# Performance work log

Measured on AMD Instinct MI355X. Metric: run time of the kernel, lower is better.

Reference implementation:

```python
import jax, jax.numpy as jnp
import numpy as np

S, T, B, E, H, V = 64, 64, 64, 256, 256, 32000
PAD = 0


def _lstm_layer(X, Wih, Whh, b, h0, c0):
    # X: (time, B, in), torch gate order i,f,g,o
    def step(carry, x_t):
        h, c = carry
        z = x_t @ Wih.T + h @ Whh.T + b
        i, f, g, o = jnp.split(z, 4, axis=-1)
        c = jax.nn.sigmoid(f) * c + jax.nn.sigmoid(i) * jnp.tanh(g)
        h = jax.nn.sigmoid(o) * jnp.tanh(c)
        return (h, c), h
    (hT, cT), outs = jax.lax.scan(step, (h0, c0), X)
    return outs, hT, cT


def setup_inputs() -> dict:
    key = jax.random.key(0)
    ks = jax.random.split(key, 20)
    p = lambda k, shape: (jax.random.normal(k, shape, jnp.float32) * 0.05)
    inp = {
        "source_padded": jax.random.randint(ks[0], (S, B), 0, V, jnp.int32),
        "target_padded": jax.random.randint(ks[1], (T, B), 0, V, jnp.int32),
        "src_emb": p(ks[2], (V, E)),
        "tgt_emb": p(ks[3], (V, E)),
        "enc_Wih_f": p(ks[4], (4 * H, E)),
        "enc_Whh_f": p(ks[5], (4 * H, H)),
        "enc_b_f": p(ks[6], (4 * H,)),
        "enc_Wih_b": p(ks[7], (4 * H, E)),
        "enc_Whh_b": p(ks[8], (4 * H, H)),
        "enc_b_b": p(ks[9], (4 * H,)),
        "dec_Wih": p(ks[10], (4 * H, E + H)),
        "dec_Whh": p(ks[11], (4 * H, H)),
        "dec_b": p(ks[12], (4 * H,)),
        "Wh": p(ks[13], (H, 2 * H)),
        "Wc": p(ks[14], (H, 2 * H)),
        "Watt": p(ks[15], (H, 2 * H)),
        "Wcomb": p(ks[16], (H, 3 * H)),
        "Wvocab": p(ks[17], (V, H)),
    }
    return inp


def reference(source_padded, target_padded, src_emb, tgt_emb,
              enc_Wih_f, enc_Whh_f, enc_b_f, enc_Wih_b, enc_Whh_b, enc_b_b,
              dec_Wih, dec_Whh, dec_b, Wh, Wc, Watt, Wcomb, Wvocab):
    X = src_emb[source_padded]                      # (S,B,E)
    h0 = jnp.zeros((B, H), X.dtype)
    c0 = jnp.zeros((B, H), X.dtype)
    # bidirectional encoder (all sequences full length -> pack is identity)
    fwd_out, hf, cf = _lstm_layer(X, enc_Wih_f, enc_Whh_f, enc_b_f, h0, c0)
    bwd_out, hb, cb = _lstm_layer(X[::-1], enc_Wih_b, enc_Whh_b, enc_b_b, h0, c0)
    bwd_out = bwd_out[::-1]
    enc_hiddens = jnp.concatenate([fwd_out, bwd_out], -1).transpose(1, 0, 2)  # (B,S,2H)
    dec_h = jnp.concatenate([hf, hb], -1) @ Wh.T     # h_projection
    dec_c = jnp.concatenate([cf, cb], -1) @ Wc.T     # c_projection
    enc_proj = enc_hiddens @ Watt.T                  # (B,S,H)

    Y = tgt_emb[target_padded[:-1]]                  # (T-1,B,E)

    def dstep(carry, Y_t):
        h, c, o_prev = carry
        x = jnp.concatenate([Y_t, o_prev], -1)       # (B,E+H)
        z = x @ dec_Wih.T + h @ dec_Whh.T + dec_b
        i, f, g, o = jnp.split(z, 4, axis=-1)
        c = jax.nn.sigmoid(f) * c + jax.nn.sigmoid(i) * jnp.tanh(g)
        h = jax.nn.sigmoid(o) * jnp.tanh(c)
        e_t = jnp.einsum('bsh,bh->bs', enc_proj, h)  # attention scores
        alpha = jax.nn.softmax(e_t, axis=-1)         # no pads -> mask is no-op
        a_t = jnp.einsum('bs,bsd->bd', alpha, enc_hiddens)  # context (B,2H)
        O_t = jnp.tanh(jnp.concatenate([a_t, h], -1) @ Wcomb.T)  # dropout=eval
        return (h, c, O_t), O_t

    _, outs = jax.lax.scan(dstep, (dec_h, dec_c, jnp.zeros((B, H), X.dtype)), Y)
    P = jax.nn.log_softmax(outs @ Wvocab.T, axis=-1)          # (T-1,B,V)
    gold = jnp.take_along_axis(P, target_padded[1:][..., None], axis=-1)[..., 0]
    tmask = (target_padded[1:] != PAD).astype(P.dtype)
    return (gold * tmask).sum(axis=0)                          # (B,)
```

## Files before the change

kernel.cpp:

```cpp
#include <hip/hip_runtime.h>
#include <hip/hip_bf16.h>

static constexpr int S = 64, T = 64, B = 64, E = 256, H = 256, V = 32000;
static constexpr int H4 = 4 * H;
static constexpr int NCHUNK = 500;
static constexpr int NROW = (T - 1) * B;
static constexpr int LDP = 264;

typedef short bf16x8 __attribute__((ext_vector_type(8)));
typedef float f32x4 __attribute__((ext_vector_type(4)));
typedef unsigned long long ull;

__device__ __forceinline__ float sigf(float x) { return 1.0f / (1.0f + __expf(-x)); }
__device__ __forceinline__ float tanhfast(float x) { return 1.0f - 2.0f / (__expf(2.0f * x) + 1.0f); }
__device__ __forceinline__ float bflo(uint w) { return __uint_as_float(w << 16); }
__device__ __forceinline__ float bfhi(uint w) { return __uint_as_float(w & 0xffff0000u); }
__device__ __forceinline__ ushort f2bu(float x) {
  return __bfloat16_as_ushort(__float2bfloat16(x));
}
__device__ __forceinline__ uint packbf(float a, float b) {
  return (uint)f2bu(a) | ((uint)f2bu(b) << 16);
}

__device__ __forceinline__ void st_u32(uint* p, uint v) {
  __hip_atomic_store(p, v, __ATOMIC_RELAXED, __HIP_MEMORY_SCOPE_AGENT);
}
__device__ __forceinline__ uint ld_u32(const uint* p) {
  return __hip_atomic_load(p, __ATOMIC_RELAXED, __HIP_MEMORY_SCOPE_AGENT);
}

__global__ __launch_bounds__(256) void k_gemm_gather(
    const int* __restrict__ idx, const float* __restrict__ emb,
    const float* __restrict__ W, int wld, const float* __restrict__ bias,
    float* __restrict__ C, int ldc) {
  __shared__ __align__(16) ushort Asl[64 * LDP];
  __shared__ __align__(16) ushort Bsl[64 * LDP];
  const int cb = blockIdx.x * 64, rb = blockIdx.y * 64;
  const int tid = threadIdx.x;
  const int lane = tid & 63, wid = tid >> 6;
  const int wr = wid >> 1, wc = wid & 1;
  const int l15 = lane & 15, l4 = lane >> 4;
  for (int it = 0; it < 8; it++) {
    int c = it * 256 + tid;
    int row = c >> 5, off = (c & 31) * 8;
    const float* asrc = emb + (size_t)idx[rb + row] * 256 + off;
    float4 a0 = *(const float4*)asrc;
    float4 a1 = *(const float4*)(asrc + 4);
    uint4 av;
    av.x = packbf(a0.x, a0.y); av.y = packbf(a0.z, a0.w);
    av.z = packbf(a1.x, a1.y); av.w = packbf(a1.z, a1.w);
    *(uint4*)&Asl[row * LDP + off] = av;
    const float* bsrc = W + (size_t)(cb + row) * wld + off;
    float4 b0 = *(const float4*)bsrc;
    float4 b1 = *(const float4*)(bsrc + 4);
    uint4 bv;
    bv.x = packbf(b0.x, b0.y); bv.y = packbf(b0.z, b0.w);
    bv.z = packbf(b1.x, b1.y); bv.w = packbf(b1.z, b1.w);
    *(uint4*)&Bsl[row * LDP + off] = bv;
  }
  __syncthreads();
  f32x4 acc[2][2];
  #pragma unroll
  for (int m = 0; m < 2; m++)
    #pragma unroll
    for (int n = 0; n < 2; n++) acc[m][n] = (f32x4){0.f, 0.f, 0.f, 0.f};
  for (int kk = 0; kk < 8; kk++) {
    int ko = kk * 32 + l4 * 8;
    bf16x8 a0 = *(const bf16x8*)&Asl[(wr * 32 + l15) * LDP + ko];
    bf16x8 a1 = *(const bf16x8*)&Asl[(wr * 32 + 16 + l15) * LDP + ko];
    bf16x8 b0 = *(const bf16x8*)&Bsl[(wc * 32 + l15) * LDP + ko];
    bf16x8 b1 = *(const bf16x8*)&Bsl[(wc * 32 + 16 + l15) * LDP + ko];
    acc[0][0] = __builtin_amdgcn_mfma_f32_16x16x32_bf16(a0, b0, acc[0][0], 0, 0, 0);
    acc[0][1] = __builtin_amdgcn_mfma_f32_16x16x32_bf16(a0, b1, acc[0][1], 0, 0, 0);
    acc[1][0] = __builtin_amdgcn_mfma_f32_16x16x32_bf16(a1, b0, acc[1][0], 0, 0, 0);
    acc[1][1] = __builtin_amdgcn_mfma_f32_16x16x32_bf16(a1, b1, acc[1][1], 0, 0, 0);
  }
  #pragma unroll
  for (int m = 0; m < 2; m++)
    #pragma unroll
    for (int n = 0; n < 2; n++) {
      int col = cb + wc * 32 + n * 16 + l15;
      float bv = bias[col];
      #pragma unroll
      for (int r = 0; r < 4; r++) {
        int row = rb + wr * 32 + m * 16 + l4 * 4 + r;
        C[(size_t)row * ldc + col] = acc[m][n][r] + bv;
      }
    }
}

__global__ __launch_bounds__(256) void k_encproj_mfma(
    const __hip_bfloat16* __restrict__ fwd_bf, const __hip_bfloat16* __restrict__ bwd_bf,
    const __hip_bfloat16* __restrict__ Watt_bf, __hip_bfloat16* __restrict__ encproj_bf) {
  __shared__ __align__(16) ushort Asl[64 * LDP];
  __shared__ __align__(16) ushort Bsl[64 * LDP];
  const int cb = blockIdx.x * 64, rb = blockIdx.y * 64;
  const int tid = threadIdx.x;
  const int lane = tid & 63, wid = tid >> 6;
  const int wr = wid >> 1, wc = wid & 1;
  const int l15 = lane & 15, l4 = lane >> 4;
  f32x4 acc[2][2];
  #pragma unroll
  for (int m = 0; m < 2; m++)
    #pragma unroll
    for (int n = 0; n < 2; n++) acc[m][n] = (f32x4){0.f, 0.f, 0.f, 0.f};
  for (int kt = 0; kt < 2; kt++) {
    if (kt) __syncthreads();
    for (int it = 0; it < 8; it++) {
      int c = it * 256 + tid;
      int row = c >> 5, off = (c & 31) * 8;
      int r = rb + row, s = r >> 6, bb = r & 63;
      const ushort* arow = (kt == 0)
          ? (const ushort*)fwd_bf + (size_t)(s * 64 + bb) * 256
          : (const ushort*)bwd_bf + (size_t)(s * 64 + bb) * 256;
      *(uint4*)&Asl[row * LDP + off] = *(const uint4*)(arow + off);
      *(uint4*)&Bsl[row * LDP + off] =
          *(const uint4*)((const ushort*)Watt_bf + (size_t)(cb + row) * 512 + kt * 256 + off);
    }
    __syncthreads();
    for (int kk = 0; kk < 8; kk++) {
      int ko = kk * 32 + l4 * 8;
      bf16x8 a0 = *(const bf16x8*)&Asl[(wr * 32 + l15) * LDP + ko];
      bf16x8 a1 = *(const bf16x8*)&Asl[(wr * 32 + 16 + l15) * LDP + ko];
      bf16x8 b0 = *(const bf16x8*)&Bsl[(wc * 32 + l15) * LDP + ko];
      bf16x8 b1 = *(const bf16x8*)&Bsl[(wc * 32 + 16 + l15) * LDP + ko];
      acc[0][0] = __builtin_amdgcn_mfma_f32_16x16x32_bf16(a0, b0, acc[0][0], 0, 0, 0);
      acc[0][1] = __builtin_amdgcn_mfma_f32_16x16x32_bf16(a0, b1, acc[0][1], 0, 0, 0);
      acc[1][0] = __builtin_amdgcn_mfma_f32_16x16x32_bf16(a1, b0, acc[1][0], 0, 0, 0);
      acc[1][1] = __builtin_amdgcn_mfma_f32_16x16x32_bf16(a1, b1, acc[1][1], 0, 0, 0);
    }
  }
  #pragma unroll
  for (int m = 0; m < 2; m++)
    #pragma unroll
    for (int n = 0; n < 2; n++) {
      int col = cb + wc * 32 + n * 16 + l15;
      #pragma unroll
      for (int r = 0; r < 4; r++) {
        int row = rb + wr * 32 + m * 16 + l4 * 4 + r;
        int s = row >> 6, bb = row & 63;
        ((ushort*)encproj_bf)[(size_t)(bb * 64 + s) * 256 + col] = f2bu(acc[m][n][r]);
      }
    }
}

__global__ __launch_bounds__(256) void k_vocab2(
    const uint* __restrict__ outs_u, const __hip_bfloat16* __restrict__ Wv,
    const int* __restrict__ tgt, float* __restrict__ part_max,
    float* __restrict__ part_sum, float* __restrict__ gold) {
  __shared__ __align__(16) ushort Asl[64 * LDP];
  __shared__ __align__(16) ushort Bsl[64 * LDP];
  __shared__ int goldcol[64];
  __shared__ float pm[64][2], ps[64][2];
  const int vb = blockIdx.x;
  const int tid = threadIdx.x;
  const int lane = tid & 63, wid = tid >> 6;
  const int wr = wid >> 1, wc = wid & 1;
  const int l15 = lane & 15, l4 = lane >> 4;
  for (int it = 0; it < 8; it++) {
    int c = it * 256 + tid;
    int row = c >> 5, off = (c & 31) * 8;
    *(uint4*)&Bsl[row * LDP + off] =
        *(const uint4*)((const ushort*)Wv + (size_t)(vb * 64 + row) * 256 + off);
  }
  for (int t = 0; t < T - 1; t++) {
    __syncthreads();
    for (int i = tid; i < 64 * 128; i += 256) {
      int row = i >> 7, colu = i & 127;
      uint v = outs_u[(size_t)(t * 64 + row) * 128 + colu];
      *(uint*)&Asl[row * LDP + colu * 2] = v;
    }
    if (tid < 64) goldcol[tid] = tgt[(t + 1) * B + tid];
    __syncthreads();
    f32x4 acc[2][2];
    #pragma unroll
    for (int m = 0; m < 2; m++)
      #pragma unroll
      for (int n = 0; n < 2; n++) acc[m][n] = (f32x4){0.f, 0.f, 0.f, 0.f};
    for (int kk = 0; kk < 8; kk++) {
      int ko = kk * 32 + l4 * 8;
      bf16x8 a0 = *(const bf16x8*)&Asl[(wr * 32 + l15) * LDP + ko];
      bf16x8 a1 = *(const bf16x8*)&Asl[(wr * 32 + 16 + l15) * LDP + ko];
      bf16x8 b0 = *(const bf16x8*)&Bsl[(wc * 32 + l15) * LDP + ko];
      bf16x8 b1 = *(const bf16x8*)&Bsl[(wc * 32 + 16 + l15) * LDP + ko];
      acc[0][0] = __builtin_amdgcn_mfma_f32_16x16x32_bf16(a0, b0, acc[0][0], 0, 0, 0);
      acc[0][1] = __builtin_amdgcn_mfma_f32_16x16x32_bf16(a0, b1, acc[0][1], 0, 0, 0);
      acc[1][0] = __builtin_amdgcn_mfma_f32_16x16x32_bf16(a1, b0, acc[1][0], 0, 0, 0);
      acc[1][1] = __builtin_amdgcn_mfma_f32_16x16x32_bf16(a1, b1, acc[1][1], 0, 0, 0);
    }
    #pragma unroll
    for (int m = 0; m < 2; m++) {
      #pragma unroll
      for (int r = 0; r < 4; r++) {
        int row_local = wr * 32 + m * 16 + l4 * 4 + r;
        int gc = goldcol[row_local];
        #pragma unroll
        for (int n = 0; n < 2; n++) {
          int col = vb * 64 + wc * 32 + n * 16 + l15;
          if (col == gc) gold[t * 64 + row_local] = acc[m][n][r];
        }
        float v = fmaxf(acc[m][0][r], acc[m][1][r]);
        #pragma unroll
        for (int o = 1; o < 16; o <<= 1) v = fmaxf(v, __shfl_xor(v, o));
        float e = __expf(acc[m][0][r] - v) + __expf(acc[m][1][r] - v);
        #pragma unroll
        for (int o = 1; o < 16; o <<= 1) e += __shfl_xor(e, o);
        if (l15 == 0) { pm[row_local][wc] = v; ps[row_local][wc] = e; }
      }
    }
    __syncthreads();
    if (tid < 64) {
      float m0 = pm[tid][0], m1 = pm[tid][1];
      float M = fmaxf(m0, m1);
      float Ss = ps[tid][0] * __expf(m0 - M) + ps[tid][1] * __expf(m1 - M);
      part_max[(size_t)vb * NROW + t * 64 + tid] = M;
      part_sum[(size_t)vb * NROW + t * 64 + tid] = Ss;
    }
  }
}

__global__ __launch_bounds__(256) void k_enc4w(
    const float* __restrict__ XwF, const float* __restrict__ XwB,
    const float* __restrict__ WhhF, const float* __restrict__ WhhB,
    uint* __restrict__ Xenc_u32,
    __hip_bfloat16* __restrict__ fwd_bf, __hip_bfloat16* __restrict__ bwd_bf,
    float* __restrict__ Cfin, uint* __restrict__ eflags,
    const float* __restrict__ Wv, __hip_bfloat16* __restrict__ Wv_bf,
    const float* __restrict__ Watt, __hip_bfloat16* __restrict__ Watt_bf,
    const float* __restrict__ Wcomb, uint2* __restrict__ Wcq) {
  __shared__ __align__(16) ushort Wl[128 * 264];
  __shared__ __align__(16) ushort Xa[16 * 264];
  __shared__ float zz[4][8][33];
  const int id = blockIdx.x;
  const int tid = threadIdx.x;
  if (id >= 128) {
    const int wtid = (id - 128) * 256 + tid;
    const int wn = 64 * 256;
    for (int i = wtid; i < (V * H) / 4; i += wn) {
      float4 v = ((const float4*)Wv)[i];
      uint2 o; o.x = packbf(v.x, v.y); o.y = packbf(v.z, v.w);
      ((uint2*)Wv_bf)[i] = o;
    }
    for (int i = wtid; i < (H * 512) / 4; i += wn) {
      float4 v = ((const float4*)Watt)[i];
      uint2 o; o.x = packbf(v.x, v.y); o.y = packbf(v.z, v.w);
      ((uint2*)Watt_bf)[i] = o;
    }
    for (int i2 = wtid; i2 < 192 * 256; i2 += wn) {
      int i = i2 >> 8, j = i2 & 255;
      float4 v = *(const float4*)(Wcomb + (size_t)j * 768 + 4 * i);
      uint2 o; o.x = packbf(v.x, v.y); o.y = packbf(v.z, v.w);
      Wcq[(size_t)i * 256 + j] = o;
    }
    return;
  }
  const int g = id & 7, kb = id >> 3;
  const int dir = kb >> 3, s = kb & 7;
  const float* Whh = dir ? WhhB : WhhF;
  const float* Xw = dir ? XwB : XwF;
  uint* fl = eflags + (size_t)(g * 2 + dir) * 8 * 32;
  for (int i = tid; i < 128 * 256; i += 256) {
    int c = i >> 8, k2 = i & 255;
    int gate = c >> 5, jj = c & 31;
    Wl[c * 264 + k2] = f2bu(Whh[(size_t)(gate * 256 + s * 32 + jj) * 256 + k2]);
  }
  for (int i = tid; i < 16 * 264; i += 256) Xa[i] = 0;
  const int lane = tid & 63, w = tid >> 6;
  const int l15 = lane & 15, l4 = lane >> 4;
  const int tb = tid >> 5, tjj = tid & 31;
  float c_reg = 0.f;
  __syncthreads();
  for (int st = 0; st < 64; st++) {
    const int ts = dir ? 63 - st : st;
    const int par = st & 1;
    const uint* Xr = Xenc_u32 + (size_t)(par * 2 + dir) * 8192;
    uint* Xo = Xenc_u32 + (size_t)((par ^ 1) * 2 + dir) * 8192;
    for (int i = tid; i < 8 * 128; i += 256) {
      int row = i >> 7, colu = i & 127;
      uint v = ld_u32(Xr + (size_t)(8 * g + row) * 128 + colu);
      *(uint*)&Xa[row * 264 + colu * 2] = v;
    }
    __syncthreads();
    f32x4 a0v = (f32x4){0.f, 0.f, 0.f, 0.f}, a1v = (f32x4){0.f, 0.f, 0.f, 0.f};
    for (int kk = 0; kk < 8; kk++) {
      bf16x8 af = *(const bf16x8*)&Xa[l15 * 264 + kk * 32 + l4 * 8];
      bf16x8 b0 = *(const bf16x8*)&Wl[((2 * w) * 16 + l15) * 264 + kk * 32 + l4 * 8];
      bf16x8 b1 = *(const bf16x8*)&Wl[((2 * w + 1) * 16 + l15) * 264 + kk * 32 + l4 * 8];
      a0v = __builtin_amdgcn_mfma_f32_16x16x32_bf16(af, b0, a0v, 0, 0, 0);
      a1v = __builtin_amdgcn_mfma_f32_16x16x32_bf16(af, b1, a1v, 0, 0, 0);
    }
    if (l4 < 2) {
      #pragma unroll
      for (int r = 0; r < 4; r++) {
        int b = l4 * 4 + r;
        zz[w][b][l15] = a0v[r];
        zz[w][b][16 + l15] = a1v[r];
      }
    }
    __syncthreads();
    {
      int gb = 8 * g + tb, j = 32 * s + tjj;
      const float* xw = Xw + (size_t)(ts * 64 + gb) * 1024;
      float zi = zz[0][tb][tjj] + xw[j];
      float zf = zz[1][tb][tjj] + xw[256 + j];
      float zg = zz[2][tb][tjj] + xw[512 + j];
      float zo = zz[3][tb][tjj] + xw[768 + j];
      float c = sigf(zf) * c_reg + sigf(zi) * tanhfast(zg);
      c_reg = c;
      float h = sigf(zo) * tanhfast(c);
      ushort hb = f2bu(h);
      if (dir == 0) ((ushort*)fwd_bf)[(size_t)(st * 64 + gb) * 256 + j] = hb;
      else          ((ushort*)bwd_bf)[(size_t)((63 - st) * 64 + gb) * 256 + j] = hb;
      float hp = __shfl_xor(h, 1);
      if ((tjj & 1) == 0)
        st_u32(Xo + (size_t)gb * 128 + 16 * s + (tjj >> 1), packbf(h, hp));
    }
    __syncthreads();
    if (tid == 0) st_u32(&fl[s * 32], (uint)(st + 1));
    if (tid < 8)
      while (ld_u32(&fl[tid * 32]) < (uint)(st + 1)) __builtin_amdgcn_s_sleep(2);
    asm volatile("" ::: "memory");
    __syncthreads();
  }
  Cfin[(size_t)(dir * 64 + 8 * g + tb) * 256 + 32 * s + tjj] = c_reg;
}

__global__ __launch_bounds__(256) void k_dec_init3(
    const __hip_bfloat16* __restrict__ Xenc, const float* __restrict__ Cfin,
    const float* __restrict__ Wh, const float* __restrict__ Wc,
    uint* __restrict__ Xd_u32, float* __restrict__ decc0) {
  int b = blockIdx.x, tid = threadIdx.x;
  __shared__ __align__(16) float ch[512], cc[512];
  __shared__ float hh[256];
  ch[tid]       = __bfloat162float(Xenc[(size_t)(0 * 64 + b) * 256 + tid]);
  ch[256 + tid] = __bfloat162float(Xenc[(size_t)(1 * 64 + b) * 256 + tid]);
  cc[tid]       = Cfin[(size_t)(0 * 64 + b) * 256 + tid];
  cc[256 + tid] = Cfin[(size_t)(1 * 64 + b) * 256 + tid];
  __syncthreads();
  const float* wh = Wh + tid * 512;
  const float* wc = Wc + tid * 512;
  float ah = 0, ac = 0;
  for (int k = 0; k < 512; k += 4) {
    float4 hv = *(const float4*)&ch[k];
    float4 cv = *(const float4*)&cc[k];
    float4 w1 = *(const float4*)&wh[k];
    float4 w2 = *(const float4*)&wc[k];
    ah += hv.x * w1.x + hv.y * w1.y + hv.z * w1.z + hv.w * w1.w;
    ac += cv.x * w2.x + cv.y * w2.y + cv.z * w2.z + cv.w * w2.w;
  }
  decc0[b * 256 + tid] = ac;
  hh[tid] = ah;
  __syncthreads();
  if (tid < 128) {
    Xd_u32[(size_t)b * 256 + tid] = packbf(hh[2 * tid], hh[2 * tid + 1]);
    Xd_u32[(size_t)b * 256 + 128 + tid] = 0u;
  }
}

__global__ __launch_bounds__(512) void k_dec6(
    const float* __restrict__ YW, const float* __restrict__ dWih,
    const float* __restrict__ dWhh, const uint2* __restrict__ Wcq,
    const __hip_bfloat16* __restrict__ encproj_bf,
    const __hip_bfloat16* __restrict__ fwd_bf, const __hip_bfloat16* __restrict__ bwd_bf,
    const float* __restrict__ decc0, uint* __restrict__ Xd_u32,
    uint* __restrict__ outs_u,
    uint* __restrict__ zflags, uint* __restrict__ aflags) {
  __shared__ __align__(16) char smem[154112];
  const int id = blockIdx.x;
  const int g = id & 7, kb = id >> 3;
  const int tid = threadIdx.x;
  uint* zfl = zflags + (size_t)g * 8 * 32;
  uint* afl = aflags + (size_t)g * 16 * 32;

  if (kb < 8) {
    const int s = kb;
    ushort* Wl = (ushort*)smem;
    ushort* Xa = (ushort*)(smem + 133120);
    float* zslds = (float*)(smem + 149760);
    for (int i = tid; i < 128 * 512; i += 512) {
      int c = i >> 9, k2 = i & 511;
      int gate = c >> 5, jj = c & 31;
      int gr = gate * 256 + 32 * s + jj;
      float v = (k2 < 256) ? dWhh[(size_t)gr * 256 + k2]
                           : dWih[(size_t)gr * 512 + 256 + (k2 - 256)];
      Wl[c * 520 + k2] = f2bu(v);
    }
    for (int i = tid; i < 16 * 520; i += 512) Xa[i] = 0;
    const int lane = tid & 63, w = tid >> 6;
    const int l15 = lane & 15, l4 = lane >> 4;
    float c_reg = 0.f;
    if (tid < 256) {
      int b = tid >> 5, jj = tid & 31;
      c_reg = decc0[(size_t)(8 * g + b) * 256 + 32 * s + jj];
    }
    __syncthreads();
    for (int i = tid; i < 8 * 128; i += 512) {
      int row = i >> 7, p = i & 127;
      uint v = ld_u32(Xd_u32 + (size_t)(8 * g + row) * 256 + p);
      *(uint*)&Xa[row * 520 + 2 * p] = v;
    }
    __syncthreads();
    f32x4 accv = (f32x4){0.f, 0.f, 0.f, 0.f};
    for (int kk = 0; kk < 8; kk++) {
      bf16x8 af = *(const bf16x8*)&Xa[l15 * 520 + kk * 32 + l4 * 8];
      bf16x8 bf = *(const bf16x8*)&Wl[(w * 16 + l15) * 520 + kk * 32 + l4 * 8];
      accv = __builtin_amdgcn_mfma_f32_16x16x32_bf16(af, bf, accv, 0, 0, 0);
    }
    for (int t = 0; t < 63; t++) {
      const int par = t & 1;
      if (t > 0) {
        if (tid < 16)
          while (ld_u32(&afl[tid * 32]) < (uint)t) __builtin_amdgcn_s_sleep(1);
        asm volatile("" ::: "memory");
        __syncthreads();
      }
      for (int i = tid; i < 8 * 128; i += 512) {
        int row = i >> 7, p = i & 127;
        uint v = ld_u32(Xd_u32 + (size_t)par * 16384 + (size_t)(8 * g + row) * 256 + 128 + p);
        *(uint*)&Xa[row * 520 + 256 + 2 * p] = v;
      }
      __syncthreads();
      for (int kk = 8; kk < 16; kk++) {
        bf16x8 af = *(const bf16x8*)&Xa[l15 * 520 + kk * 32 + l4 * 8];
        bf16x8 bf = *(const bf16x8*)&Wl[(w * 16 + l15) * 520 + kk * 32 + l4 * 8];
        accv = __builtin_amdgcn_mfma_f32_16x16x32_bf16(af, bf, accv, 0, 0, 0);
      }
      if (l4 < 2) {
        #pragma unroll
        for (int r = 0; r < 4; r++) {
          int b = l4 * 4 + r;
          zslds[b * 128 + w * 16 + l15] = accv[r];
        }
      }
      __syncthreads();
      if (tid < 256) {
        int b = tid >> 5, jj = tid & 31;
        int gb = 8 * g + b;
        const float* yw = YW + (size_t)(t * 64 + gb) * 1024 + 32 * s + jj;
        float zi = zslds[b * 128 + jj] + yw[0];
        float zf = zslds[b * 128 + 32 + jj] + yw[256];
        float zg = zslds[b * 128 + 64 + jj] + yw[512];
        float zo = zslds[b * 128 + 96 + jj] + yw[768];
        float c = sigf(zf) * c_reg + sigf(zi) * tanhfast(zg);
        c_reg = c;
        float h = sigf(zo) * tanhfast(c);
        float hp = __shfl_xor(h, 1);
        if ((jj & 1) == 0)
          st_u32(Xd_u32 + (size_t)(par ^ 1) * 16384 + (size_t)gb * 256 + 16 * s + (jj >> 1),
                 packbf(h, hp));
      }
      __syncthreads();
      if (tid == 0) st_u32(&zfl[s * 32], (uint)(t + 1));
      if (t < 62) {
        if (tid < 8)
          while (ld_u32(&zfl[tid * 32]) < (uint)(t + 1)) __builtin_amdgcn_s_sleep(1);
        asm volatile("" ::: "memory");
        __syncthreads();
        for (int i = tid; i < 8 * 128; i += 512) {
          int row = i >> 7, p = i & 127;
          uint v = ld_u32(Xd_u32 + (size_t)(par ^ 1) * 16384 + (size_t)(8 * g + row) * 256 + p);
          *(uint*)&Xa[row * 520 + 2 * p] = v;
        }
        __syncthreads();
        accv = (f32x4){0.f, 0.f, 0.f, 0.f};
        for (int kk = 0; kk < 8; kk++) {
          bf16x8 af = *(const bf16x8*)&Xa[l15 * 520 + kk * 32 + l4 * 8];
          bf16x8 bf = *(const bf16x8*)&Wl[(w * 16 + l15) * 520 + kk * 32 + l4 * 8];
          accv = __builtin_amdgcn_mfma_f32_16x16x32_bf16(af, bf, accv, 0, 0, 0);
        }
      }
    }
  } else {
    const int lb = (kb - 8) >> 1, jh = (kb - 8) & 1;
    const int b = 8 * g + lb;
    ushort* ep = (ushort*)smem;
    ushort* eh = (ushort*)(smem + 33792);
    float* hn = (float*)(smem + 100352);
    float* xcomb = (float*)(smem + 101376);
    float* e_l = (float*)(smem + 104448);
    float* alpha_l = (float*)(smem + 104704);
    float* op_l = (float*)(smem + 104960);
    for (int i = tid; i < 64 * 256; i += 512) {
      int s2 = i >> 8, k2 = i & 255;
      ep[s2 * 264 + k2] = ((const ushort*)encproj_bf)[(size_t)(b * 64 + s2) * 256 + k2];
    }
    for (int i = tid; i < 64 * 512; i += 512) {
      int s2 = i >> 9, d = i & 511;
      ushort v = (d < 256) ? ((const ushort*)fwd_bf)[(size_t)(s2 * 64 + b) * 256 + d]
                           : ((const ushort*)bwd_bf)[(size_t)(s2 * 64 + b) * 256 + d - 256];
      eh[s2 * 520 + d] = v;
    }
    __syncthreads();
    for (int t = 0; t < 63; t++) {
      if (tid < 8)
        while (ld_u32(&zfl[tid * 32]) < (uint)(t + 1)) __builtin_amdgcn_s_sleep(1);
      asm volatile("" ::: "memory");
      __syncthreads();
      if (tid < 128) {
        uint v = ld_u32(Xd_u32 + (size_t)((t & 1) ^ 1) * 16384 + (size_t)b * 256 + tid);
        hn[2 * tid] = bflo(v);
        hn[2 * tid + 1] = bfhi(v);
      }
      __syncthreads();
      {
        int s2 = tid >> 3, q8 = tid & 7;
        const ushort* pr = ep + s2 * 264 + q8 * 32;
        const float* hq = hn + q8 * 32;
        float a = 0.f;
        #pragma unroll 8
        for (int kk = 0; kk < 32; kk += 2) {
          uint wv = *(const uint*)(pr + kk);
          a += bflo(wv) * hq[kk] + bfhi(wv) * hq[kk + 1];
        }
        a += __shfl_xor(a, 1);
        a += __shfl_xor(a, 2);
        a += __shfl_xor(a, 4);
        if (q8 == 0) e_l[s2] = a;
      }
      __syncthreads();
      if (tid < 64) {
        float e = e_l[tid];
        float mx = e;
        #pragma unroll
        for (int o = 32; o > 0; o >>= 1) mx = fmaxf(mx, __shfl_xor(mx, o));
        float p = __expf(e - mx);
        float ss = p;
        #pragma unroll
        for (int o = 32; o > 0; o >>= 1) ss += __shfl_xor(ss, o);
        alpha_l[tid] = p / ss;
      }
      __syncthreads();
      {
        float a = 0.f;
        const ushort* col = eh + tid;
        #pragma unroll 8
        for (int s2 = 0; s2 < 64; s2++)
          a += alpha_l[s2] * __uint_as_float(((uint)col[s2 * 520]) << 16);
        xcomb[tid] = a;
        if (tid < 256) xcomb[512 + tid] = hn[tid];
      }
      __syncthreads();
      {
        int jl = tid & 127, kq = tid >> 7;
        int j = jh * 128 + jl;
        const uint2* wp = Wcq + (size_t)(kq * 48) * 256 + j;
        const float4* x4 = (const float4*)xcomb + kq * 48;
        float a = 0.f;
        #pragma unroll 6
        for (int ii = 0; ii < 48; ii++) {
          uint2 wv = wp[(size_t)ii * 256];
          float4 xv = x4[ii];
          a += bflo(wv.x) * xv.x + bfhi(wv.x) * xv.y + bflo(wv.y) * xv.z + bfhi(wv.y) * xv.w;
        }
        op_l[kq * 128 + jl] = a;
      }
      __syncthreads();
      if (tid < 128) {
        float sum = op_l[tid] + op_l[128 + tid] + op_l[256 + tid] + op_l[384 + tid];
        float O = tanhfast(sum);
        float Op = __shfl_xor(O, 1);
        if ((tid & 1) == 0) {
          uint v = packbf(O, Op);
          st_u32(Xd_u32 + (size_t)((t & 1) ^ 1) * 16384 + (size_t)b * 256 + 128 + jh * 64 + (tid >> 1), v);
          st_u32(outs_u + (size_t)(t * 64 + b) * 128 + jh * 64 + (tid >> 1), v);
        }
      }
      __syncthreads();
      if (tid == 0) st_u32(&afl[(lb * 2 + jh) * 32], (uint)(t + 1));
    }
  }
}

__global__ __launch_bounds__(256) void k_final(
    const float* __restrict__ part_max, const float* __restrict__ part_sum,
    const float* __restrict__ gold, const int* __restrict__ tgt,
    float* __restrict__ out) {
  int b = blockIdx.x, tid = threadIdx.x;
  int tq = tid >> 2, q = tid & 3;
  __shared__ float lm[64][4], ls[64][4];
  __shared__ float red[64];
  if (tq < T - 1) {
    int n = tq * B + b;
    float m = -__builtin_inff(), s = 0;
    for (int i = q; i < NCHUNK; i += 4) {
      float pmv = part_max[(size_t)i * NROW + n];
      float psv = part_sum[(size_t)i * NROW + n];
      float M2 = fmaxf(m, pmv);
      s = s * __expf(m - M2) + psv * __expf(pmv - M2);
      m = M2;
    }
    lm[tq][q] = m;
    ls[tq][q] = s;
  }
  __syncthreads();
  if (tid < T - 1) {
    float M = fmaxf(fmaxf(lm[tid][0], lm[tid][1]), fmaxf(lm[tid][2], lm[tid][3]));
    float Ss = ls[tid][0] * __expf(lm[tid][0] - M) + ls[tid][1] * __expf(lm[tid][1] - M) +
               ls[tid][2] * __expf(lm[tid][2] - M) + ls[tid][3] * __expf(lm[tid][3] - M);
    float lse = M + logf(Ss);
    int g = tgt[(tid + 1) * B + b];
    red[tid] = (g != 0) ? (gold[tid * B + b] - lse) : 0.f;
  }
  if (tid == T - 1) red[T - 1] = 0.f;
  __syncthreads();
  if (tid == 0) {
    float s = 0;
    for (int i = 0; i < T - 1; i++) s += red[i];
    out[b] = s;
  }
}

extern "C" void kernel_launch(void* const* d_in, const int* in_sizes, int n_in,
                              void* d_out, int out_size, void* d_ws, size_t ws_size,
                              hipStream_t stream) {
  (void)in_sizes; (void)n_in; (void)out_size; (void)ws_size;
  const int*   src   = (const int*)  d_in[0];
  const int*   tgt   = (const int*)  d_in[1];
  const float* semb  = (const float*)d_in[2];
  const float* temb  = (const float*)d_in[3];
  const float* WihF  = (const float*)d_in[4];
  const float* WhhF  = (const float*)d_in[5];
  const float* bF    = (const float*)d_in[6];
  const float* WihB  = (const float*)d_in[7];
  const float* WhhB  = (const float*)d_in[8];
  const float* bB    = (const float*)d_in[9];
  const float* dWih  = (const float*)d_in[10];
  const float* dWhh  = (const float*)d_in[11];
  const float* db    = (const float*)d_in[12];
  const float* Wh    = (const float*)d_in[13];
  const float* Wc    = (const float*)d_in[14];
  const float* Watt  = (const float*)d_in[15];
  const float* Wcomb = (const float*)d_in[16];
  const float* Wv    = (const float*)d_in[17];
  float* out = (float*)d_out;

  char* wp = (char*)d_ws;
  auto alloc = [&](size_t bytes) -> char* {
    char* p = wp;
    wp += (bytes + 255) & ~(size_t)255;
    return p;
  };
  float* XwF  = (float*)alloc((size_t)S * B * H4 * 4);
  float* XwB  = (float*)alloc((size_t)S * B * H4 * 4);
  float* YW   = (float*)alloc((size_t)(T - 1) * B * H4 * 4);
  __hip_bfloat16* fwd_bf     = (__hip_bfloat16*)alloc((size_t)S * B * H * 2);
  __hip_bfloat16* bwd_bf     = (__hip_bfloat16*)alloc((size_t)S * B * H * 2);
  __hip_bfloat16* encproj_bf = (__hip_bfloat16*)alloc((size_t)B * S * H * 2);
  __hip_bfloat16* Wv_bf      = (__hip_bfloat16*)alloc((size_t)V * H * 2);
  __hip_bfloat16* Watt_bf    = (__hip_bfloat16*)alloc((size_t)H * 512 * 2);
  uint* outs_u = (uint*)alloc((size_t)NROW * H * 2);
  uint2* Wcq = (uint2*)alloc((size_t)192 * 256 * 8);
  float* part_max = (float*)alloc((size_t)NCHUNK * NROW * 4);
  float* part_sum = (float*)alloc((size_t)NCHUNK * NROW * 4);
  float* gold     = (float*)alloc((size_t)NROW * 4);
  float* Cfin  = (float*)alloc((size_t)2 * B * H * 4);
  float* decc0 = (float*)alloc((size_t)B * H * 4);
  __hip_bfloat16* Xenc = (__hip_bfloat16*)alloc((size_t)2 * 2 * B * H * 2);
  uint* Xdec = (uint*)alloc((size_t)2 * B * 256 * 4);
  char* stateBase = wp;
  uint* eflags = (uint*)alloc(16 * 8 * 32 * 4);
  uint* zflags = (uint*)alloc(8 * 8 * 32 * 4);
  uint* aflags = (uint*)alloc(8 * 16 * 32 * 4);
  size_t stateBytes = (size_t)(wp - stateBase);
  hipMemsetAsync(stateBase, 0, stateBytes, stream);
  hipMemsetAsync(Xenc, 0, (size_t)2 * 2 * B * H * 2, stream);

  hipLaunchKernelGGL(k_gemm_gather, dim3(16, 64), dim3(256), 0, stream,
                     src, semb, WihF, 256, bF, XwF, H4);
  hipLaunchKernelGGL(k_gemm_gather, dim3(16, 64), dim3(256), 0, stream,
                     src, semb, WihB, 256, bB, XwB, H4);

  hipLaunchKernelGGL(k_enc4w, dim3(192), dim3(256), 0, stream,
                     XwF, XwB, WhhF, WhhB, (uint*)Xenc, fwd_bf, bwd_bf, Cfin, eflags,
                     Wv, Wv_bf, Watt, Watt_bf, Wcomb, Wcq);

  hipLaunchKernelGGL(k_gemm_gather, dim3(16, 63), dim3(256), 0, stream,
                     tgt, temb, dWih, 512, db, YW, H4);
  hipLaunchKernelGGL(k_dec_init3, dim3(B), dim3(256), 0, stream,
                     Xenc, Cfin, Wh, Wc, Xdec, decc0);
  hipLaunchKernelGGL(k_encproj_mfma, dim3(4, 64), dim3(256), 0, stream,
                     fwd_bf, bwd_bf, Watt_bf, encproj_bf);

  hipLaunchKernelGGL(k_dec6, dim3(192), dim3(512), 0, stream,
                     YW, dWih, dWhh, Wcq, encproj_bf, fwd_bf, bwd_bf,
                     decc0, Xdec, outs_u, zflags, aflags);

  hipLaunchKernelGGL(k_vocab2, dim3(NCHUNK), dim3(256), 0, stream,
                     outs_u, Wv_bf, tgt, part_max, part_sum, gold);
  hipLaunchKernelGGL(k_final, dim3(B), dim3(256), 0, stream,
                     part_max, part_sum, gold, tgt, out);
}
```

Before: 1.230 ms.

## Overlap decoder input GEMM with encoder recurrence and split Wcomb h-part earlier

The target-embedding input GEMM (YW) used to be its own launch after the encoder. It now runs inside the 64 idle weight-conversion blocks of the encoder kernel, so it overlaps the serial encoder recurrence and one launch is removed. In the decoder step, the Wcomb product with h is computed by half the threads in the same phase as the attention scores. The remaining Wcomb pass then only covers the 512-wide context, which shortens the serial chain per step. The cost is more shared memory in the encoder kernel and extra work for the helper blocks, which could delay the bf16 weight conversions.

```diff
diff --git a/kernel.cpp b/kernel.cpp
--- a/kernel.cpp
+++ b/kernel.cpp
@@ -29,13 +29,11 @@
   return __hip_atomic_load(p, __ATOMIC_RELAXED, __HIP_MEMORY_SCOPE_AGENT);
 }
 
-__global__ __launch_bounds__(256) void k_gemm_gather(
+__device__ void gemm_gather_tile(
     const int* __restrict__ idx, const float* __restrict__ emb,
     const float* __restrict__ W, int wld, const float* __restrict__ bias,
-    float* __restrict__ C, int ldc) {
-  __shared__ __align__(16) ushort Asl[64 * LDP];
-  __shared__ __align__(16) ushort Bsl[64 * LDP];
-  const int cb = blockIdx.x * 64, rb = blockIdx.y * 64;
+    float* __restrict__ C, int ldc, int cb, int rb,
+    ushort* Asl, ushort* Bsl) {
   const int tid = threadIdx.x;
   const int lane = tid & 63, wid = tid >> 6;
   const int wr = wid >> 1, wc = wid & 1;
@@ -87,6 +85,17 @@
         C[(size_t)row * ldc + col] = acc[m][n][r] + bv;
       }
     }
+  __syncthreads();
+}
+
+__global__ __launch_bounds__(256) void k_gemm_gather(
+    const int* __restrict__ idx, const float* __restrict__ emb,
+    const float* __restrict__ W, int wld, const float* __restrict__ bias,
+    float* __restrict__ C, int ldc) {
+  __shared__ __align__(16) ushort Asl[64 * LDP];
+  __shared__ __align__(16) ushort Bsl[64 * LDP];
+  gemm_gather_tile(idx, emb, W, wld, bias, C, ldc,
+                   blockIdx.x * 64, blockIdx.y * 64, Asl, Bsl);
 }
 
 __global__ __launch_bounds__(256) void k_encproj_mfma(
@@ -227,14 +236,23 @@
     float* __restrict__ Cfin, uint* __restrict__ eflags,
     const float* __restrict__ Wv, __hip_bfloat16* __restrict__ Wv_bf,
     const float* __restrict__ Watt, __hip_bfloat16* __restrict__ Watt_bf,
-    const float* __restrict__ Wcomb, uint2* __restrict__ Wcq) {
-  __shared__ __align__(16) ushort Wl[128 * 264];
-  __shared__ __align__(16) ushort Xa[16 * 264];
+    const float* __restrict__ Wcomb, uint2* __restrict__ Wcq,
+    const int* __restrict__ tgt, const float* __restrict__ temb,
+    const float* __restrict__ dWih, const float* __restrict__ db,
+    float* __restrict__ YW) {
+  __shared__ __align__(16) char smem[80256];
   __shared__ float zz[4][8][33];
   const int id = blockIdx.x;
   const int tid = threadIdx.x;
   if (id >= 128) {
-    const int wtid = (id - 128) * 256 + tid;
+    ushort* Asl = (ushort*)smem;
+    ushort* Bsl = (ushort*)(smem + 33792);
+    const int wb = id - 128;
+    for (int tau = wb; tau < 16 * 63; tau += 64) {
+      int cb = (tau & 15) * 64, rb = (tau >> 4) * 64;
+      gemm_gather_tile(tgt, temb, dWih, 512, db, YW, H4, cb, rb, Asl, Bsl);
+    }
+    const int wtid = wb * 256 + tid;
     const int wn = 64 * 256;
     for (int i = wtid; i < (V * H) / 4; i += wn) {
       float4 v = ((const float4*)Wv)[i];
@@ -254,6 +272,8 @@
     }
     return;
   }
+  ushort* Wl = (ushort*)smem;
+  ushort* Xa = (ushort*)(smem + 67584);
   const int g = id & 7, kb = id >> 3;
   const int dir = kb >> 3, s = kb & 7;
   const float* Whh = dir ? WhhB : WhhF;
@@ -357,7 +377,7 @@
   }
 }
 
-__global__ __launch_bounds__(512) void k_dec6(
+__global__ __launch_bounds__(512) void k_dec7(
     const float* __restrict__ YW, const float* __restrict__ dWih,
     const float* __restrict__ dWhh, const uint2* __restrict__ Wcq,
     const __hip_bfloat16* __restrict__ encproj_bf,
@@ -480,6 +500,7 @@
     float* e_l = (float*)(smem + 104448);
     float* alpha_l = (float*)(smem + 104704);
     float* op_l = (float*)(smem + 104960);
+    float* ophh = (float*)(smem + 107008);
     for (int i = tid; i < 64 * 256; i += 512) {
       int s2 = i >> 8, k2 = i & 255;
       ep[s2 * 264 + k2] = ((const ushort*)encproj_bf)[(size_t)(b * 64 + s2) * 256 + k2];
@@ -502,20 +523,33 @@
         hn[2 * tid + 1] = bfhi(v);
       }
       __syncthreads();
-      {
-        int s2 = tid >> 3, q8 = tid & 7;
-        const ushort* pr = ep + s2 * 264 + q8 * 32;
-        const float* hq = hn + q8 * 32;
+      if (tid < 256) {
+        int s2 = tid >> 2, q4 = tid & 3;
+        const ushort* pr = ep + s2 * 264 + q4 * 64;
+        const float* hq = hn + q4 * 64;
         float a = 0.f;
         #pragma unroll 8
-        for (int kk = 0; kk < 32; kk += 2) {
+        for (int kk = 0; kk < 64; kk += 2) {
           uint wv = *(const uint*)(pr + kk);
           a += bflo(wv) * hq[kk] + bfhi(wv) * hq[kk + 1];
         }
         a += __shfl_xor(a, 1);
         a += __shfl_xor(a, 2);
-        a += __shfl_xor(a, 4);
-        if (q8 == 0) e_l[s2] = a;
+        if (q4 == 0) e_l[s2] = a;
+      } else {
+        int u = tid - 256;
+        int jl = u >> 1, hf = u & 1;
+        int j = jh * 128 + jl;
+        const uint2* wp = Wcq + (size_t)(128 + hf * 32) * 256 + j;
+        const float4* h4 = (const float4*)hn + hf * 32;
+        float a = 0.f;
+        #pragma unroll 8
+        for (int ii = 0; ii < 32; ii++) {
+          uint2 wv = wp[(size_t)ii * 256];
+          float4 xv = h4[ii];
+          a += bflo(wv.x) * xv.x + bfhi(wv.x) * xv.y + bflo(wv.y) * xv.z + bfhi(wv.y) * xv.w;
+        }
+        ophh[hf * 128 + jl] = a;
       }
       __syncthreads();
       if (tid < 64) {
@@ -537,17 +571,16 @@
         for (int s2 = 0; s2 < 64; s2++)
           a += alpha_l[s2] * __uint_as_float(((uint)col[s2 * 520]) << 16);
         xcomb[tid] = a;
-        if (tid < 256) xcomb[512 + tid] = hn[tid];
       }
       __syncthreads();
       {
         int jl = tid & 127, kq = tid >> 7;
         int j = jh * 128 + jl;
-        const uint2* wp = Wcq + (size_t)(kq * 48) * 256 + j;
-        const float4* x4 = (const float4*)xcomb + kq * 48;
+        const uint2* wp = Wcq + (size_t)(kq * 32) * 256 + j;
+        const float4* x4 = (const float4*)xcomb + kq * 32;
         float a = 0.f;
-        #pragma unroll 6
-        for (int ii = 0; ii < 48; ii++) {
+        #pragma unroll 8
+        for (int ii = 0; ii < 32; ii++) {
           uint2 wv = wp[(size_t)ii * 256];
           float4 xv = x4[ii];
           a += bflo(wv.x) * xv.x + bfhi(wv.x) * xv.y + bflo(wv.y) * xv.z + bfhi(wv.y) * xv.w;
@@ -556,7 +589,8 @@
       }
       __syncthreads();
       if (tid < 128) {
-        float sum = op_l[tid] + op_l[128 + tid] + op_l[256 + tid] + op_l[384 + tid];
+        float sum = op_l[tid] + op_l[128 + tid] + op_l[256 + tid] + op_l[384 + tid]
+                  + ophh[tid] + ophh[128 + tid];
         float O = tanhfast(sum);
         float Op = __shfl_xor(O, 1);
         if ((tid & 1) == 0) {
@@ -672,16 +706,15 @@
 
   hipLaunchKernelGGL(k_enc4w, dim3(192), dim3(256), 0, stream,
                      XwF, XwB, WhhF, WhhB, (uint*)Xenc, fwd_bf, bwd_bf, Cfin, eflags,
-                     Wv, Wv_bf, Watt, Watt_bf, Wcomb, Wcq);
-
-  hipLaunchKernelGGL(k_gemm_gather, dim3(16, 63), dim3(256), 0, stream,
-                     tgt, temb, dWih, 512, db, YW, H4);
+                     Wv, Wv_bf, Watt, Watt_bf, Wcomb, Wcq,
+                     tgt, temb, dWih, db, YW);
+
   hipLaunchKernelGGL(k_dec_init3, dim3(B), dim3(256), 0, stream,
                      Xenc, Cfin, Wh, Wc, Xdec, decc0);
   hipLaunchKernelGGL(k_encproj_mfma, dim3(4, 64), dim3(256), 0, stream,
                      fwd_bf, bwd_bf, Watt_bf, encproj_bf);
 
-  hipLaunchKernelGGL(k_dec6, dim3(192), dim3(512), 0, stream,
+  hipLaunchKernelGGL(k_dec7, dim3(192), dim3(512), 0, stream,
                      YW, dWih, dWhh, Wcq, encproj_bf, fwd_bf, bwd_bf,
                      decc0, Xdec, outs_u, zflags, aflags);
 
```

Measured after the change: 1.246 ms. No clear change (+1.3%).
